# Kernel tuning notes

Measured on AMD Instinct MI355X. Metric: run time of the kernel, lower is better.

Reference implementation:

```python
import jax, jax.numpy as jnp
import numpy as np

DIM = 1152
N_HEADS = 12
GROUPS = 6
KV_HEADS = N_HEADS // GROUPS  # 2
HEAD_DIM = DIM // N_HEADS     # 96
BASE = 10000.0
BSZ = 4
SEQ = 2048
MAX_SEQ = 2048
NEG_INF = -1e9


def rope(x, start_pos):
    # x: [b, s, h, d]; interleaved (even/odd) rotary embedding, matching the torch code
    b, s, h, d = x.shape
    x_even = x[..., 0::2]
    x_odd = x[..., 1::2]
    # even positions <- -x_odd, odd positions <- x_even (interleaved)
    x_rev = jnp.stack([-x_odd, x_even], axis=-1).reshape(x.shape)
    i = jnp.repeat(jnp.arange(0, d, 2), 2).astype(x.dtype)  # [d]
    theta = 1.0 / (BASE ** (i / d))                          # [d]
    pos = jnp.arange(start_pos + s, dtype=x.dtype)           # [s] (start_pos=0 case, as in source)
    ang = pos[:, None] * theta[None, :]                      # [s, d]
    cos = jnp.cos(ang).reshape(1, s, 1, d)
    sin = jnp.sin(ang).reshape(1, s, 1, d)
    return x * cos + x_rev * sin


def setup_inputs() -> dict:
    key = jax.random.key(0)
    ks = jax.random.split(key, 4)
    sc = 0.02
    x = jax.random.normal(ks[0], (BSZ, SEQ, DIM), jnp.float32)
    # causal mask [S, end_pos]: 0 on/below diagonal, large negative above
    mask = jnp.triu(jnp.full((SEQ, SEQ), NEG_INF, jnp.float32), k=1)
    q_w = jax.random.normal(ks[1], (DIM, DIM), jnp.float32) * sc
    q_b = jnp.zeros((DIM,), jnp.float32)
    kv_w = jax.random.normal(ks[2], (2 * KV_HEADS * HEAD_DIM, DIM), jnp.float32) * sc
    kv_b = jnp.zeros((2 * KV_HEADS * HEAD_DIM,), jnp.float32)
    wo_w = jax.random.normal(ks[3], (DIM, DIM), jnp.float32) * sc
    wo_b = jnp.zeros((DIM,), jnp.float32)
    return {"x": x, "mask": mask, "q_w": q_w, "q_b": q_b, "kv_w": kv_w,
            "kv_b": kv_b, "wo_w": wo_w, "wo_b": wo_b, "start_pos": 0}


def reference(x, mask, q_w, q_b, kv_w, kv_b, wo_w, wo_b, start_pos):
    b, s, f = x.shape
    end = start_pos + s
    q = (x @ q_w.T + q_b).reshape(b, s, N_HEADS, HEAD_DIM)
    kv = (x @ kv_w.T + kv_b).reshape(b, s, 2, KV_HEADS, HEAD_DIM)
    k, v = kv[:, :, 0], kv[:, :, 1]
    rq = rope(q, start_pos)
    rk = rope(k, start_pos)
    # KV-cache write (cache initialized to zeros, as in the buffer)
    k_cache = jnp.zeros((b, MAX_SEQ, KV_HEADS, HEAD_DIM), x.dtype).at[:, start_pos:end].set(rk)
    v_cache = jnp.zeros((b, MAX_SEQ, KV_HEADS, HEAD_DIM), x.dtype).at[:, start_pos:end].set(v)
    # repeat_kv: head index = kv_head * groups + g  -> jnp.repeat along head axis
    kk = jnp.repeat(k_cache[:, :end], GROUPS, axis=2)  # [b, t, H, d]
    vv = jnp.repeat(v_cache[:, :end], GROUPS, axis=2)
    scale = HEAD_DIM ** -0.5
    attn = jnp.einsum('bshd,bthd->bsht', rq, kk) * scale
    attn = attn + mask[:, None, :]  # mask [s, t] -> [s, 1, t] broadcast over b, h
    scores = jax.nn.softmax(attn.astype(jnp.float32), axis=-1).astype(x.dtype)
    out = jnp.einsum('bsht,bthd->bshd', scores, vv).reshape(b, s, DIM)
    return out @ wo_w.T + wo_b
```

## Files before the change

kernel.cpp:

```cpp
#include <hip/hip_runtime.h>
#include <hip/hip_bf16.h>

constexpr int DIMD  = 1152;
constexpr int NHD   = 12;
constexpr int KVHD  = 2;
constexpr int HDD   = 96;
constexpr int GRPS  = 6;
constexpr int SEQL  = 2048;
constexpr int BSZ4  = 4;
constexpr int MROWS = BSZ4 * SEQL;
constexpr int NQKV  = DIMD + 2 * KVHD * HDD;
constexpr float SCALE = 0.10206207261596577f;
constexpr float SCALE2 = 0.10206207261596577f * 1.4426950408889634f;

typedef short  bf16x8 __attribute__((ext_vector_type(8)));
typedef float  f32x4  __attribute__((ext_vector_type(4)));

typedef __attribute__((address_space(3))) unsigned int       lds_u32_t;
typedef __attribute__((address_space(1))) const unsigned int glb_u32_t;

__device__ __forceinline__ void gload16(const unsigned short* g, unsigned short* l) {
    __builtin_amdgcn_global_load_lds((glb_u32_t*)(const void*)g,
                                     (lds_u32_t*)(void*)l, 16, 0, 0);
}

__device__ __forceinline__ unsigned short f2bf(float f) {
    unsigned int u = __builtin_bit_cast(unsigned int, f);
    u += 0x7fff + ((u >> 16) & 1);
    return (unsigned short)(u >> 16);
}

__device__ __forceinline__ unsigned cvtpk(float a, float b) {
    unsigned r;
    asm volatile("v_cvt_pk_bf16_f32 %0, %1, %2" : "=v"(r) : "v"(a), "v"(b));
    return r;
}

__device__ __forceinline__ float ex2(float x) {
    float r;
    asm volatile("v_exp_f32 %0, %1" : "=v"(r) : "v"(x));
    return r;
}

__device__ __forceinline__ void cvt4(const float4* __restrict__ s,
                                     ushort4* __restrict__ d, int i) {
    float4 f = s[i];
    ushort4 o;
    o.x = f2bf(f.x); o.y = f2bf(f.y); o.z = f2bf(f.z); o.w = f2bf(f.w);
    d[i] = o;
}

__global__ __launch_bounds__(256) void prep_kernel(
    const float4* __restrict__ x,   const float4* __restrict__ qw,
    const float4* __restrict__ kvw, const float4* __restrict__ wow,
    ushort4* __restrict__ xb,   ushort4* __restrict__ qwb,
    ushort4* __restrict__ kvwb, ushort4* __restrict__ wowb,
    const int* __restrict__ sp, float2* __restrict__ tab)
{
    constexpr int X4  = MROWS * DIMD / 4;
    constexpr int W4  = DIMD * DIMD / 4;
    constexpr int KV4 = 2 * KVHD * HDD * DIMD / 4;
    constexpr int NT  = SEQL * 48;
    int i = blockIdx.x * 256 + threadIdx.x;
    if (i < X4)  { cvt4(x, xb, i); return; }
    i -= X4;
    if (i < W4)  { cvt4(qw, qwb, i); return; }
    i -= W4;
    if (i < KV4) { cvt4(kvw, kvwb, i); return; }
    i -= KV4;
    if (i < W4)  { cvt4(wow, wowb, i); return; }
    i -= W4;
    if (i < NT) {
        int s = i / 48, j = i - (i / 48) * 48;
        float th = powf(10000.0f, -(float)(2 * j) / 96.0f);
        float ang = (float)(s + *sp) * th;
        float sn, cs; sincosf(ang, &sn, &cs);
        tab[i] = make_float2(cs, sn);
    }
}

__global__ __launch_bounds__(256) void qkv_mfma_kernel(
    const unsigned short* __restrict__ xb,  const unsigned short* __restrict__ qwb,
    const unsigned short* __restrict__ kvwb,
    const float* __restrict__ qb,  const float* __restrict__ kvb,
    const float2* __restrict__ tab,
    unsigned short* __restrict__ Qo, unsigned short* __restrict__ Ko,
    unsigned short* __restrict__ VTo)
{
    __shared__ __align__(16) unsigned short As[3][128 * 32];
    __shared__ __align__(16) unsigned short Bs[3][128 * 32];

    const int tid  = threadIdx.x;
    const int w    = tid >> 6;
    const int lane = tid & 63;
    const int l16  = lane & 15;
    const int quad = lane >> 4;
    const int wm   = w >> 1, wn = w & 1;

    const int flat = (int)(blockIdx.y * gridDim.x + blockIdx.x);
    const int swz  = (flat & 7) * 96 + (flat >> 3);
    const int m0   = (swz / 12) * 128;
    const int n0   = (swz % 12) * 128;

    const unsigned short* Abase = xb + (size_t)m0 * DIMD;
    const unsigned short* Bbase = (n0 < DIMD)
        ? qwb  + (size_t)n0 * DIMD
        : kvwb + (size_t)(n0 - DIMD) * DIMD;

    const int srow = w * 16 + (lane >> 2);
    const int scol = (lane & 3) * 8;

    f32x4 acc[4][4];
    #pragma unroll
    for (int mi = 0; mi < 4; mi++)
        #pragma unroll
        for (int ni = 0; ni < 4; ni++) acc[mi][ni] = (f32x4){0.f, 0.f, 0.f, 0.f};

    constexpr int NK = DIMD / 32;

    gload16(Abase + (size_t)srow        * DIMD + scol, &As[0][w * 512]);
    gload16(Abase + (size_t)(srow + 64) * DIMD + scol, &As[0][2048 + w * 512]);
    gload16(Bbase + (size_t)srow        * DIMD + scol, &Bs[0][w * 512]);
    gload16(Bbase + (size_t)(srow + 64) * DIMD + scol, &Bs[0][2048 + w * 512]);
    gload16(Abase + (size_t)srow        * DIMD + 32 + scol, &As[1][w * 512]);
    gload16(Abase + (size_t)(srow + 64) * DIMD + 32 + scol, &As[1][2048 + w * 512]);
    gload16(Bbase + (size_t)srow        * DIMD + 32 + scol, &Bs[1][w * 512]);
    gload16(Bbase + (size_t)(srow + 64) * DIMD + 32 + scol, &Bs[1][2048 + w * 512]);

    for (int kt = 0; kt < NK; kt++) {
        const int cur = kt % 3;
        if (kt + 2 < NK) {
            const int stg = (kt + 2) % 3;
            const int k0  = (kt + 2) * 32;
            gload16(Abase + (size_t)srow        * DIMD + k0 + scol, &As[stg][w * 512]);
            gload16(Abase + (size_t)(srow + 64) * DIMD + k0 + scol, &As[stg][2048 + w * 512]);
            gload16(Bbase + (size_t)srow        * DIMD + k0 + scol, &Bs[stg][w * 512]);
            gload16(Bbase + (size_t)(srow + 64) * DIMD + k0 + scol, &Bs[stg][2048 + w * 512]);
            asm volatile("s_waitcnt vmcnt(8)" ::: "memory");
        } else if (kt + 1 < NK) {
            asm volatile("s_waitcnt vmcnt(4)" ::: "memory");
        } else {
            asm volatile("s_waitcnt vmcnt(0)" ::: "memory");
        }
        __builtin_amdgcn_s_barrier();
        asm volatile("" ::: "memory");

        bf16x8 af[4], bfr[4];
        #pragma unroll
        for (int mi = 0; mi < 4; mi++)
            af[mi] = *(const bf16x8*)&As[cur][(wm * 64 + mi * 16 + l16) * 32 + quad * 8];
        #pragma unroll
        for (int ni = 0; ni < 4; ni++)
            bfr[ni] = *(const bf16x8*)&Bs[cur][(wn * 64 + ni * 16 + l16) * 32 + quad * 8];
        #pragma unroll
        for (int mi = 0; mi < 4; mi++)
            #pragma unroll
            for (int ni = 0; ni < 4; ni++)
                acc[mi][ni] = __builtin_amdgcn_mfma_f32_16x16x32_bf16(
                    af[mi], bfr[ni], acc[mi][ni], 0, 0, 0);

        asm volatile("" ::: "memory");
        __builtin_amdgcn_s_barrier();
    }

    #pragma unroll
    for (int ni = 0; ni < 4; ni++) {
        const int n   = n0 + wn * 64 + ni * 16 + l16;
        const bool isQ = (n < DIMD);
        const int jj  = n - DIMD;
        const bool isK = !isQ && (jj < KVHD * HDD);
        const int d   = isQ ? (n % HDD) : (jj % HDD);
        const int hh  = isQ ? (n / HDD) : ((jj / HDD) & 1);
        const float bias = isQ ? qb[n] : kvb[jj];
        const bool doRope = isQ || isK;
        const int de2 = (d >> 1);
        const float sg = (n & 1) ? 1.0f : -1.0f;
        #pragma unroll
        for (int mi = 0; mi < 4; mi++) {
            #pragma unroll
            for (int r = 0; r < 4; r++) {
                const int m = m0 + wm * 64 + mi * 16 + quad * 4 + r;
                const int b = m >> 11;
                const int s = m & (SEQL - 1);
                float v  = acc[mi][ni][r] + bias;
                float pv = __shfl_xor(v, 1, 64);
                float o = v;
                if (doRope) {
                    float2 cs2 = tab[s * 48 + de2];
                    o = v * cs2.x + sg * pv * cs2.y;
                }
                if (isQ)
                    Qo[(((size_t)b * NHD + hh) * SEQL + s) * HDD + d] = f2bf(o);
                else if (isK)
                    Ko[(((size_t)b * KVHD + hh) * SEQL + s) * HDD + d] = f2bf(o);
                else
                    VTo[(((size_t)b * KVHD + hh) * HDD + d) * SEQL + s] = f2bf(o);
            }
        }
    }
}

__global__ __launch_bounds__(256, 3) void attn_mfma_kernel(
    const unsigned short* __restrict__ Q, const unsigned short* __restrict__ K,
    const unsigned short* __restrict__ VT, unsigned short* __restrict__ AO)
{
    constexpr int KHALF = 64 * 104;
    __shared__ __align__(16) unsigned short Ks[2 * KHALF];
    __shared__ __align__(16) unsigned short VTs[96 * 72];
    __shared__ __align__(16) unsigned short Ps[4][16 * 72];
    __shared__ float Al[4][16];

    const int tid  = threadIdx.x;
    const int w    = tid >> 6;
    const int lane = tid & 63;
    const int l16  = lane & 15;
    const int quad = lane >> 4;

    const int idx  = (int)blockIdx.x;
    const int grp  = idx & 7;
    const int j    = idx >> 3;
    const int jq   = j / 6;
    const int hrem = j - jq * 6;
    const int qt   = 31 - jq;
    const int b    = grp >> 1;
    const int kvh  = grp & 1;
    const int h    = kvh * GRPS + hrem;
    const int nkb  = qt + 1;

    const unsigned short* Qbase  = Q  + (((size_t)b * NHD  + h)   * SEQL) * HDD;
    const unsigned short* Kbase  = K  + (((size_t)b * KVHD + kvh) * SEQL) * HDD;
    const unsigned short* VTbase = VT + (((size_t)b * KVHD + kvh) * HDD)  * SEQL;

    int goff[7]; int gkind[7]; int loff[7];
    #pragma unroll
    for (int jj = 0; jj < 7; jj++) {
        const int i = w + 4 * jj;
        gkind[jj] = 2; goff[jj] = 0; loff[jj] = 0;
        if (i < 13) {
            int slot = i * 64 + lane;
            int r = slot / 13, g = slot - r * 13;
            goff[jj]  = r * HDD + (g < 12 ? g * 8 : 0);
            gkind[jj] = 0;
            loff[jj]  = i * 512;
        } else if (i < 27) {
            int iv = i - 13;
            int slot = iv * 64 + lane;
            if (slot < 864) {
                int r = slot / 9, g = slot - r * 9;
                goff[jj]  = r * SEQL + (g < 8 ? g * 8 : 0);
                gkind[jj] = 1;
                loff[jj]  = iv * 512;
            }
        }
    }

    bf16x8 qf[3];
    {
        const int qrow = qt * 64 + w * 16 + l16;
        const unsigned short* qp = Qbase + (size_t)qrow * HDD + quad * 8;
        qf[0] = *(const bf16x8*)(qp);
        qf[1] = *(const bf16x8*)(qp + 32);
        qf[2] = *(const bf16x8*)(qp + 64);
    }

    float m_r = -1e30f, l_r = 0.0f;
    f32x4 oacc[6];
    #pragma unroll
    for (int nn = 0; nn < 6; nn++) oacc[nn] = (f32x4){0.f, 0.f, 0.f, 0.f};

    #pragma unroll
    for (int jj = 0; jj < 7; jj++)
        if (gkind[jj] == 0)
            gload16(Kbase + goff[jj], &Ks[loff[jj]]);
    #pragma unroll
    for (int jj = 0; jj < 7; jj++)
        if (gkind[jj] == 1) {
            if ((w + 4 * jj) < 26 || lane < 32)
                gload16(VTbase + goff[jj], &VTs[loff[jj]]);
        }

    const int dql = w * 16 + l16;

    for (int kb = 0; kb < nkb; kb++) {
        const int  cur  = kb & 1;
        const bool more = (kb + 1 < nkb);

        if (more) {
            const size_t kg = (size_t)(kb + 1) * 64 * HDD;
            #pragma unroll
            for (int jj = 0; jj < 7; jj++)
                if (gkind[jj] == 0)
                    gload16(Kbase + kg + goff[jj], &Ks[(cur ^ 1) * KHALF + loff[jj]]);
            asm volatile("s_waitcnt vmcnt(6)" ::: "memory");
        } else {
            asm volatile("s_waitcnt vmcnt(3)" ::: "memory");
        }
        __builtin_amdgcn_s_barrier();
        asm volatile("" ::: "memory");

        const unsigned short* ksb = &Ks[cur * KHALF];
        f32x4 s[4];
        __builtin_amdgcn_s_setprio(1);
        #pragma unroll
        for (int n = 0; n < 4; n++) {
            const unsigned short* kr = ksb + (n * 16 + l16) * 104 + quad * 8;
            bf16x8 kf0 = *(const bf16x8*)(kr);
            bf16x8 kf1 = *(const bf16x8*)(kr + 32);
            bf16x8 kf2 = *(const bf16x8*)(kr + 64);
            f32x4 a = (f32x4){0.f, 0.f, 0.f, 0.f};
            a = __builtin_amdgcn_mfma_f32_16x16x32_bf16(kf0, qf[0], a, 0, 0, 0);
            a = __builtin_amdgcn_mfma_f32_16x16x32_bf16(kf1, qf[1], a, 0, 0, 0);
            a = __builtin_amdgcn_mfma_f32_16x16x32_bf16(kf2, qf[2], a, 0, 0, 0);
            s[n] = a;
        }
        __builtin_amdgcn_s_setprio(0);

        float v[4][4];
        float mx = -3e30f;
        if (!more) {
            #pragma unroll
            for (int n = 0; n < 4; n++)
                #pragma unroll
                for (int r = 0; r < 4; r++) {
                    float x = s[n][r] * SCALE2;
                    if (n * 16 + quad * 4 + r > dql) x = -1e30f;
                    v[n][r] = x;
                    mx = fmaxf(mx, x);
                }
        } else {
            #pragma unroll
            for (int n = 0; n < 4; n++)
                #pragma unroll
                for (int r = 0; r < 4; r++) {
                    float x = s[n][r] * SCALE2;
                    v[n][r] = x;
                    mx = fmaxf(mx, x);
                }
        }
        mx = fmaxf(mx, __shfl_xor(mx, 16, 64));
        mx = fmaxf(mx, __shfl_xor(mx, 32, 64));

        const bool resc = !__all(mx <= m_r + 8.0f);
        float mnew = m_r, al = 1.0f;
        if (resc) {
            mnew = fmaxf(m_r, mx);
            al = ex2(m_r - mnew);
            if (quad == 0) Al[w][l16] = al;
        }
        float sum = 0.0f;
        #pragma unroll
        for (int n = 0; n < 4; n++) {
            float p0 = ex2(v[n][0] - mnew);
            float p1 = ex2(v[n][1] - mnew);
            float p2 = ex2(v[n][2] - mnew);
            float p3 = ex2(v[n][3] - mnew);
            sum += (p0 + p1) + (p2 + p3);
            uint2 pk;
            pk.x = cvtpk(p0, p1);
            pk.y = cvtpk(p2, p3);
            *(uint2*)&Ps[w][l16 * 72 + n * 16 + quad * 4] = pk;
        }
        sum += __shfl_xor(sum, 16, 64);
        sum += __shfl_xor(sum, 32, 64);
        l_r = l_r * al + sum;
        m_r = mnew;
        __builtin_amdgcn_wave_barrier();

        bf16x8 pa0 = *(const bf16x8*)&Ps[w][l16 * 72 + quad * 8];
        bf16x8 pa1 = *(const bf16x8*)&Ps[w][l16 * 72 + 32 + quad * 8];

        if (more) asm volatile("s_waitcnt vmcnt(3)" ::: "memory");
        else      asm volatile("s_waitcnt vmcnt(0)" ::: "memory");
        __builtin_amdgcn_s_barrier();
        asm volatile("" ::: "memory");

        if (resc) {
            const float4 alb = *(const float4*)&Al[w][quad * 4];
            const float albr[4] = {alb.x, alb.y, alb.z, alb.w};
            #pragma unroll
            for (int nn = 0; nn < 6; nn++)
                #pragma unroll
                for (int r = 0; r < 4; r++) oacc[nn][r] *= albr[r];
        }

        __builtin_amdgcn_s_setprio(1);
        #pragma unroll
        for (int nn = 0; nn < 6; nn++) {
            const unsigned short* vr = &VTs[(nn * 16 + l16) * 72 + quad * 8];
            bf16x8 vb0 = *(const bf16x8*)(vr);
            bf16x8 vb1 = *(const bf16x8*)(vr + 32);
            f32x4 a = oacc[nn];
            a = __builtin_amdgcn_mfma_f32_16x16x32_bf16(pa0, vb0, a, 0, 0, 0);
            a = __builtin_amdgcn_mfma_f32_16x16x32_bf16(pa1, vb1, a, 0, 0, 0);
            oacc[nn] = a;
        }
        __builtin_amdgcn_s_setprio(0);

        asm volatile("" ::: "memory");
        __builtin_amdgcn_s_barrier();
        asm volatile("" ::: "memory");

        if (more) {
            const int kg = (kb + 1) * 64;
            #pragma unroll
            for (int jj = 0; jj < 7; jj++)
                if (gkind[jj] == 1) {
                    if ((w + 4 * jj) < 26 || lane < 32)
                        gload16(VTbase + kg + goff[jj], &VTs[loff[jj]]);
                }
        }
    }

    const float linv = 1.0f / l_r;
    if (quad == 0) Al[w][l16] = linv;
    __builtin_amdgcn_wave_barrier();
    const float4 lb4 = *(const float4*)&Al[w][quad * 4];
    const float lbr[4] = {lb4.x, lb4.y, lb4.z, lb4.w};
    const int row0 = qt * 64 + w * 16 + quad * 4;
    #pragma unroll
    for (int nn = 0; nn < 6; nn++) {
        #pragma unroll
        for (int r = 0; r < 4; r++) {
            AO[((size_t)b * SEQL + row0 + r) * DIMD + h * HDD + nn * 16 + l16] =
                f2bf(oacc[nn][r] * lbr[r]);
        }
    }
}

__global__ __launch_bounds__(256) void out_mfma_kernel(
    const unsigned short* __restrict__ Ab, const unsigned short* __restrict__ Wb,
    const float* __restrict__ wob, float* __restrict__ out)
{
    __shared__ __align__(16) unsigned short As[3][128 * 32];
    __shared__ __align__(16) unsigned short Bs[3][128 * 32];

    const int tid  = threadIdx.x;
    const int w    = tid >> 6;
    const int lane = tid & 63;
    const int l16  = lane & 15;
    const int quad = lane >> 4;
    const int wm   = w >> 1, wn = w & 1;

    const int flat = (int)(blockIdx.y * gridDim.x + blockIdx.x);
    const int swz  = (flat & 7) * 72 + (flat >> 3);
    const int m0   = (swz / 9) * 128;
    const int n0   = (swz % 9) * 128;

    const unsigned short* Abase = Ab + (size_t)m0 * DIMD;
    const unsigned short* Bbase = Wb + (size_t)n0 * DIMD;

    const int srow = w * 16 + (lane >> 2);
    const int scol = (lane & 3) * 8;

    f32x4 acc[4][4];
    #pragma unroll
    for (int mi = 0; mi < 4; mi++)
        #pragma unroll
        for (int ni = 0; ni < 4; ni++) acc[mi][ni] = (f32x4){0.f, 0.f, 0.f, 0.f};

    constexpr int NK = DIMD / 32;

    gload16(Abase + (size_t)srow        * DIMD + scol, &As[0][w * 512]);
    gload16(Abase + (size_t)(srow + 64) * DIMD + scol, &As[0][2048 + w * 512]);
    gload16(Bbase + (size_t)srow        * DIMD + scol, &Bs[0][w * 512]);
    gload16(Bbase + (size_t)(srow + 64) * DIMD + scol, &Bs[0][2048 + w * 512]);
    gload16(Abase + (size_t)srow        * DIMD + 32 + scol, &As[1][w * 512]);
    gload16(Abase + (size_t)(srow + 64) * DIMD + 32 + scol, &As[1][2048 + w * 512]);
    gload16(Bbase + (size_t)srow        * DIMD + 32 + scol, &Bs[1][w * 512]);
    gload16(Bbase + (size_t)(srow + 64) * DIMD + 32 + scol, &Bs[1][2048 + w * 512]);

    for (int kt = 0; kt < NK; kt++) {
        const int cur = kt % 3;
        if (kt + 2 < NK) {
            const int stg = (kt + 2) % 3;
            const int k0  = (kt + 2) * 32;
            gload16(Abase + (size_t)srow        * DIMD + k0 + scol, &As[stg][w * 512]);
            gload16(Abase + (size_t)(srow + 64) * DIMD + k0 + scol, &As[stg][2048 + w * 512]);
            gload16(Bbase + (size_t)srow        * DIMD + k0 + scol, &Bs[stg][w * 512]);
            gload16(Bbase + (size_t)(srow + 64) * DIMD + k0 + scol, &Bs[stg][2048 + w * 512]);
            asm volatile("s_waitcnt vmcnt(8)" ::: "memory");
        } else if (kt + 1 < NK) {
            asm volatile("s_waitcnt vmcnt(4)" ::: "memory");
        } else {
            asm volatile("s_waitcnt vmcnt(0)" ::: "memory");
        }
        __builtin_amdgcn_s_barrier();
        asm volatile("" ::: "memory");

        bf16x8 af[4], bfr[4];
        #pragma unroll
        for (int mi = 0; mi < 4; mi++)
            af[mi] = *(const bf16x8*)&As[cur][(wm * 64 + mi * 16 + l16) * 32 + quad * 8];
        #pragma unroll
        for (int ni = 0; ni < 4; ni++)
            bfr[ni] = *(const bf16x8*)&Bs[cur][(wn * 64 + ni * 16 + l16) * 32 + quad * 8];
        #pragma unroll
        for (int mi = 0; mi < 4; mi++)
            #pragma unroll
            for (int ni = 0; ni < 4; ni++)
                acc[mi][ni] = __builtin_amdgcn_mfma_f32_16x16x32_bf16(
                    af[mi], bfr[ni], acc[mi][ni], 0, 0, 0);

        asm volatile("" ::: "memory");
        __builtin_amdgcn_s_barrier();
    }

    #pragma unroll
    for (int ni = 0; ni < 4; ni++) {
        const int n = n0 + wn * 64 + ni * 16 + l16;
        const float bias = wob[n];
        #pragma unroll
        for (int mi = 0; mi < 4; mi++) {
            #pragma unroll
            for (int r = 0; r < 4; r++) {
                const int m = m0 + wm * 64 + mi * 16 + quad * 4 + r;
                out[(size_t)m * DIMD + n] = acc[mi][ni][r] + bias;
            }
        }
    }
}

extern "C" void kernel_launch(void* const* d_in, const int* in_sizes, int n_in,
                              void* d_out, int out_size, void* d_ws, size_t ws_size,
                              hipStream_t stream)
{
    const float* x   = (const float*)d_in[0];
    const float* qw  = (const float*)d_in[2];
    const float* qb  = (const float*)d_in[3];
    const float* kvw = (const float*)d_in[4];
    const float* kvb = (const float*)d_in[5];
    const float* wow = (const float*)d_in[6];
    const float* wob = (const float*)d_in[7];
    const int*   sp  = (const int*)d_in[8];

    const size_t xN   = (size_t)MROWS * DIMD;
    const size_t qwN  = (size_t)DIMD * DIMD;
    const size_t kvwN = (size_t)2 * KVHD * HDD * DIMD;
    const size_t qN   = (size_t)BSZ4 * NHD  * SEQL * HDD;
    const size_t kvN  = (size_t)BSZ4 * KVHD * SEQL * HDD;

    unsigned short* xb   = (unsigned short*)d_ws;
    unsigned short* qwb  = xb   + xN;
    unsigned short* kvwb = qwb  + qwN;
    unsigned short* wowb = kvwb + kvwN;
    unsigned short* Q16  = wowb + qwN;
    unsigned short* K16  = Q16  + qN;
    unsigned short* VT16 = K16  + kvN;
    unsigned short* AO16 = VT16 + kvN;
    float2* tab = (float2*)AO16;

    constexpr int PREP_TOT = (MROWS * DIMD + 2 * DIMD * DIMD
                              + 2 * KVHD * HDD * DIMD) / 4 + SEQL * 48;
    prep_kernel<<<(PREP_TOT + 255) / 256, 256, 0, stream>>>(
        (const float4*)x, (const float4*)qw, (const float4*)kvw, (const float4*)wow,
        (ushort4*)xb, (ushort4*)qwb, (ushort4*)kvwb, (ushort4*)wowb, sp, tab);

    qkv_mfma_kernel<<<dim3(NQKV / 128, MROWS / 128, 1), 256, 0, stream>>>(
        xb, qwb, kvwb, qb, kvb, tab, Q16, K16, VT16);
    attn_mfma_kernel<<<dim3((SEQL / 64) * NHD * BSZ4, 1, 1), 256, 0, stream>>>(
        Q16, K16, VT16, AO16);
    out_mfma_kernel<<<dim3(DIMD / 128, MROWS / 128, 1), 256, 0, stream>>>(
        AO16, wowb, wob, (float*)d_out);
}
```

Before: 284.8 us.

## Switch attention to 32x32x16 MFMA with split-K waves and register P

Rewrites the attention inner loop to use 32x32x16 bf16 MFMAs. Each pair of waves shares a 32-row query slice and splits the 64-key block into two 32-key halves; a wave whose half lies entirely above the causal diagonal skips its work. P is repacked into MFMA operand layout in registers with cross-lane shuffles instead of going through LDS. The two halves' partial softmax states and outputs are merged at the end through LDS, which adds an epilogue reduction and extra synchronisation. It also raises register pressure under the 3-blocks-per-CU launch bound.

After: 285.1 us, median of 2. About the same (+0.1%).

```diff
diff --git a/kernel.cpp b/kernel.cpp
--- a/kernel.cpp
+++ b/kernel.cpp
@@ -15,6 +15,8 @@
 
 typedef short  bf16x8 __attribute__((ext_vector_type(8)));
 typedef float  f32x4  __attribute__((ext_vector_type(4)));
+typedef float  f32x16 __attribute__((ext_vector_type(16)));
+typedef unsigned int u32x4_t __attribute__((ext_vector_type(4)));
 
 typedef __attribute__((address_space(3))) unsigned int       lds_u32_t;
 typedef __attribute__((address_space(1))) const unsigned int glb_u32_t;
@@ -207,20 +209,22 @@
     constexpr int KHALF = 64 * 104;
     __shared__ __align__(16) unsigned short Ks[2 * KHALF];
     __shared__ __align__(16) unsigned short VTs[96 * 72];
-    __shared__ __align__(16) unsigned short Ps[4][16 * 72];
-    __shared__ float Al[4][16];
+    __shared__ float Al[4][32];
 
     const int tid  = threadIdx.x;
     const int w    = tid >> 6;
     const int lane = tid & 63;
-    const int l16  = lane & 15;
-    const int quad = lane >> 4;
+    const int l31  = lane & 31;
+    const int hi   = lane >> 5;
+    const int qh   = w >> 1;
+    const int th   = w & 1;
+    const int th32 = th * 32;
 
     const int idx  = (int)blockIdx.x;
     const int grp  = idx & 7;
-    const int j    = idx >> 3;
-    const int jq   = j / 6;
-    const int hrem = j - jq * 6;
+    const int j0   = idx >> 3;
+    const int jq   = j0 / 6;
+    const int hrem = j0 - jq * 6;
     const int qt   = 31 - jq;
     const int b    = grp >> 1;
     const int kvh  = grp & 1;
@@ -254,19 +258,20 @@
         }
     }
 
-    bf16x8 qf[3];
+    const int qv = qt * 64 + qh * 32;
+    bf16x8 qf[6];
     {
-        const int qrow = qt * 64 + w * 16 + l16;
-        const unsigned short* qp = Qbase + (size_t)qrow * HDD + quad * 8;
-        qf[0] = *(const bf16x8*)(qp);
-        qf[1] = *(const bf16x8*)(qp + 32);
-        qf[2] = *(const bf16x8*)(qp + 64);
+        const unsigned short* qp = Qbase + (size_t)(qv + l31) * HDD + hi * 8;
+        #pragma unroll
+        for (int ks = 0; ks < 6; ks++) qf[ks] = *(const bf16x8*)(qp + ks * 16);
     }
 
     float m_r = -1e30f, l_r = 0.0f;
-    f32x4 oacc[6];
-    #pragma unroll
-    for (int nn = 0; nn < 6; nn++) oacc[nn] = (f32x4){0.f, 0.f, 0.f, 0.f};
+    f32x16 oacc[3];
+    #pragma unroll
+    for (int nn = 0; nn < 3; nn++)
+        #pragma unroll
+        for (int r = 0; r < 16; r++) oacc[nn][r] = 0.0f;
 
     #pragma unroll
     for (int jj = 0; jj < 7; jj++)
@@ -279,11 +284,11 @@
                 gload16(VTbase + goff[jj], &VTs[loff[jj]]);
         }
 
-    const int dql = w * 16 + l16;
-
     for (int kb = 0; kb < nkb; kb++) {
         const int  cur  = kb & 1;
         const bool more = (kb + 1 < nkb);
+        const int  k0   = kb * 64;
+        const bool active = (k0 + th32 <= qv + 31);
 
         if (more) {
             const size_t kg = (size_t)(kb + 1) * 64 * HDD;
@@ -298,103 +303,107 @@
         __builtin_amdgcn_s_barrier();
         asm volatile("" ::: "memory");
 
-        const unsigned short* ksb = &Ks[cur * KHALF];
-        f32x4 s[4];
-        __builtin_amdgcn_s_setprio(1);
-        #pragma unroll
-        for (int n = 0; n < 4; n++) {
-            const unsigned short* kr = ksb + (n * 16 + l16) * 104 + quad * 8;
-            bf16x8 kf0 = *(const bf16x8*)(kr);
-            bf16x8 kf1 = *(const bf16x8*)(kr + 32);
-            bf16x8 kf2 = *(const bf16x8*)(kr + 64);
-            f32x4 a = (f32x4){0.f, 0.f, 0.f, 0.f};
-            a = __builtin_amdgcn_mfma_f32_16x16x32_bf16(kf0, qf[0], a, 0, 0, 0);
-            a = __builtin_amdgcn_mfma_f32_16x16x32_bf16(kf1, qf[1], a, 0, 0, 0);
-            a = __builtin_amdgcn_mfma_f32_16x16x32_bf16(kf2, qf[2], a, 0, 0, 0);
-            s[n] = a;
-        }
-        __builtin_amdgcn_s_setprio(0);
-
-        float v[4][4];
-        float mx = -3e30f;
-        if (!more) {
-            #pragma unroll
-            for (int n = 0; n < 4; n++)
-                #pragma unroll
-                for (int r = 0; r < 4; r++) {
-                    float x = s[n][r] * SCALE2;
-                    if (n * 16 + quad * 4 + r > dql) x = -1e30f;
-                    v[n][r] = x;
-                    mx = fmaxf(mx, x);
-                }
-        } else {
-            #pragma unroll
-            for (int n = 0; n < 4; n++)
-                #pragma unroll
-                for (int r = 0; r < 4; r++) {
-                    float x = s[n][r] * SCALE2;
-                    v[n][r] = x;
-                    mx = fmaxf(mx, x);
-                }
-        }
-        mx = fmaxf(mx, __shfl_xor(mx, 16, 64));
-        mx = fmaxf(mx, __shfl_xor(mx, 32, 64));
-
-        const bool resc = !__all(mx <= m_r + 8.0f);
-        float mnew = m_r, al = 1.0f;
-        if (resc) {
-            mnew = fmaxf(m_r, mx);
-            al = ex2(m_r - mnew);
-            if (quad == 0) Al[w][l16] = al;
-        }
-        float sum = 0.0f;
-        #pragma unroll
-        for (int n = 0; n < 4; n++) {
-            float p0 = ex2(v[n][0] - mnew);
-            float p1 = ex2(v[n][1] - mnew);
-            float p2 = ex2(v[n][2] - mnew);
-            float p3 = ex2(v[n][3] - mnew);
-            sum += (p0 + p1) + (p2 + p3);
-            uint2 pk;
-            pk.x = cvtpk(p0, p1);
-            pk.y = cvtpk(p2, p3);
-            *(uint2*)&Ps[w][l16 * 72 + n * 16 + quad * 4] = pk;
-        }
-        sum += __shfl_xor(sum, 16, 64);
-        sum += __shfl_xor(sum, 32, 64);
-        l_r = l_r * al + sum;
-        m_r = mnew;
-        __builtin_amdgcn_wave_barrier();
-
-        bf16x8 pa0 = *(const bf16x8*)&Ps[w][l16 * 72 + quad * 8];
-        bf16x8 pa1 = *(const bf16x8*)&Ps[w][l16 * 72 + 32 + quad * 8];
+        bf16x8 pa[2];
+        bool resc = false;
+
+        if (active) {
+            const unsigned short* ksb = &Ks[cur * KHALF + th32 * 104];
+            f32x16 s;
+            #pragma unroll
+            for (int r = 0; r < 16; r++) s[r] = 0.0f;
+            __builtin_amdgcn_s_setprio(1);
+            #pragma unroll
+            for (int ks = 0; ks < 6; ks++) {
+                bf16x8 kf = *(const bf16x8*)&ksb[l31 * 104 + ks * 16 + hi * 8];
+                s = __builtin_amdgcn_mfma_f32_32x32x16_bf16(kf, qf[ks], s, 0, 0, 0);
+            }
+            __builtin_amdgcn_s_setprio(0);
+
+            const int qabs = qv + l31;
+            float p[16];
+            float mx = -3e30f;
+            const bool domask = (k0 + th32 + 31 > qv);
+            #pragma unroll
+            for (int r = 0; r < 16; r++) {
+                const int tl = (r & 3) + 8 * (r >> 2) + 4 * hi;
+                float x = s[r] * SCALE2;
+                if (domask && (k0 + th32 + tl > qabs)) x = -1e30f;
+                p[r] = x;
+                mx = fmaxf(mx, x);
+            }
+            mx = fmaxf(mx, __shfl_xor(mx, 32, 64));
+
+            resc = !__all(mx <= m_r + 8.0f);
+            float mnew = m_r, al = 1.0f;
+            if (resc) {
+                mnew = fmaxf(m_r, mx);
+                al = ex2(m_r - mnew);
+                if (hi == 0) Al[w][l31] = al;
+            }
+            float sum = 0.0f;
+            #pragma unroll
+            for (int r = 0; r < 16; r++) {
+                p[r] = ex2(p[r] - mnew);
+                sum += p[r];
+            }
+            sum += __shfl_xor(sum, 32, 64);
+            l_r = l_r * al + sum;
+            m_r = mnew;
+
+            #pragma unroll
+            for (int tk = 0; tk < 2; tk++) {
+                const int base = tk * 8;
+                unsigned pkA0 = cvtpk(p[base + 0], p[base + 1]);
+                unsigned pkA1 = cvtpk(p[base + 2], p[base + 3]);
+                unsigned pkB0 = cvtpk(p[base + 4], p[base + 5]);
+                unsigned pkB1 = cvtpk(p[base + 6], p[base + 7]);
+                unsigned S0 = hi ? pkA0 : pkB0;
+                unsigned S1 = hi ? pkA1 : pkB1;
+                unsigned R0 = __shfl_xor(S0, 32, 64);
+                unsigned R1 = __shfl_xor(S1, 32, 64);
+                u32x4_t wv;
+                wv[0] = hi ? R0 : pkA0;
+                wv[1] = hi ? R1 : pkA1;
+                wv[2] = hi ? pkB0 : R0;
+                wv[3] = hi ? pkB1 : R1;
+                pa[tk] = __builtin_bit_cast(bf16x8, wv);
+            }
+        }
 
         if (more) asm volatile("s_waitcnt vmcnt(3)" ::: "memory");
         else      asm volatile("s_waitcnt vmcnt(0)" ::: "memory");
         __builtin_amdgcn_s_barrier();
         asm volatile("" ::: "memory");
 
-        if (resc) {
-            const float4 alb = *(const float4*)&Al[w][quad * 4];
-            const float albr[4] = {alb.x, alb.y, alb.z, alb.w};
-            #pragma unroll
-            for (int nn = 0; nn < 6; nn++)
+        if (active) {
+            if (resc) {
+                const float4 a0 = *(const float4*)&Al[w][hi * 4];
+                const float4 a1 = *(const float4*)&Al[w][8 + hi * 4];
+                const float4 a2 = *(const float4*)&Al[w][16 + hi * 4];
+                const float4 a3 = *(const float4*)&Al[w][24 + hi * 4];
+                const float ab[16] = {a0.x, a0.y, a0.z, a0.w,
+                                      a1.x, a1.y, a1.z, a1.w,
+                                      a2.x, a2.y, a2.z, a2.w,
+                                      a3.x, a3.y, a3.z, a3.w};
                 #pragma unroll
-                for (int r = 0; r < 4; r++) oacc[nn][r] *= albr[r];
-        }
-
-        __builtin_amdgcn_s_setprio(1);
-        #pragma unroll
-        for (int nn = 0; nn < 6; nn++) {
-            const unsigned short* vr = &VTs[(nn * 16 + l16) * 72 + quad * 8];
-            bf16x8 vb0 = *(const bf16x8*)(vr);
-            bf16x8 vb1 = *(const bf16x8*)(vr + 32);
-            f32x4 a = oacc[nn];
-            a = __builtin_amdgcn_mfma_f32_16x16x32_bf16(pa0, vb0, a, 0, 0, 0);
-            a = __builtin_amdgcn_mfma_f32_16x16x32_bf16(pa1, vb1, a, 0, 0, 0);
-            oacc[nn] = a;
-        }
-        __builtin_amdgcn_s_setprio(0);
+                for (int nn = 0; nn < 3; nn++)
+                    #pragma unroll
+                    for (int r = 0; r < 16; r++) oacc[nn][r] *= ab[r];
+            }
+
+            __builtin_amdgcn_s_setprio(1);
+            #pragma unroll
+            for (int nn = 0; nn < 3; nn++) {
+                const unsigned short* vr = &VTs[(nn * 32 + l31) * 72 + th32 + hi * 8];
+                bf16x8 vb0 = *(const bf16x8*)(vr);
+                bf16x8 vb1 = *(const bf16x8*)(vr + 16);
+                f32x16 a = oacc[nn];
+                a = __builtin_amdgcn_mfma_f32_32x32x16_bf16(pa[0], vb0, a, 0, 0, 0);
+                a = __builtin_amdgcn_mfma_f32_32x32x16_bf16(pa[1], vb1, a, 0, 0, 0);
+                oacc[nn] = a;
+            }
+            __builtin_amdgcn_s_setprio(0);
+        }
 
         asm volatile("" ::: "memory");
         __builtin_amdgcn_s_barrier();
@@ -411,19 +420,60 @@
         }
     }
 
-    const float linv = 1.0f / l_r;
-    if (quad == 0) Al[w][l16] = linv;
-    __builtin_amdgcn_wave_barrier();
-    const float4 lb4 = *(const float4*)&Al[w][quad * 4];
-    const float lbr[4] = {lb4.x, lb4.y, lb4.z, lb4.w};
-    const int row0 = qt * 64 + w * 16 + quad * 4;
-    #pragma unroll
-    for (int nn = 0; nn < 6; nn++) {
-        #pragma unroll
-        for (int r = 0; r < 4; r++) {
-            AO[((size_t)b * SEQL + row0 + r) * DIMD + h * HDD + nn * 16 + l16] =
-                f2bf(oacc[nn][r] * lbr[r]);
-        }
+    __syncthreads();
+    float* Mx  = (float*)VTs;
+    float* Lx  = Mx + 128;
+    float* Gs  = Lx + 128;
+    float* Osc = (float*)Ks;
+    if (hi == 0) { Mx[w * 32 + l31] = m_r; Lx[w * 32 + l31] = l_r; }
+    __syncthreads();
+    {
+        const int wp = w ^ 1;
+        const float m_p = Mx[wp * 32 + l31];
+        const float l_p = Lx[wp * 32 + l31];
+        const float mm  = fmaxf(m_r, m_p);
+        const float fs  = ex2(m_r - mm);
+        const float lt  = l_r * fs + l_p * ex2(m_p - mm);
+        if (hi == 0) Gs[w * 32 + l31] = fs / lt;
+    }
+    __syncthreads();
+    float gr[16];
+    {
+        const float4 a0 = *(const float4*)&Gs[w * 32 + hi * 4];
+        const float4 a1 = *(const float4*)&Gs[w * 32 + 8 + hi * 4];
+        const float4 a2 = *(const float4*)&Gs[w * 32 + 16 + hi * 4];
+        const float4 a3 = *(const float4*)&Gs[w * 32 + 24 + hi * 4];
+        gr[0]  = a0.x; gr[1]  = a0.y; gr[2]  = a0.z; gr[3]  = a0.w;
+        gr[4]  = a1.x; gr[5]  = a1.y; gr[6]  = a1.z; gr[7]  = a1.w;
+        gr[8]  = a2.x; gr[9]  = a2.y; gr[10] = a2.z; gr[11] = a2.w;
+        gr[12] = a3.x; gr[13] = a3.y; gr[14] = a3.z; gr[15] = a3.w;
+    }
+    #pragma unroll
+    for (int nn = 0; nn < 3; nn++)
+        #pragma unroll
+        for (int r = 0; r < 16; r++) oacc[nn][r] *= gr[r];
+
+    if (th == 1) {
+        #pragma unroll
+        for (int nn = 0; nn < 3; nn++)
+            #pragma unroll
+            for (int r = 0; r < 16; r++) {
+                const int ql = (r & 3) + 8 * (r >> 2) + 4 * hi;
+                Osc[(qh * 32 + ql) * 96 + nn * 32 + l31] = oacc[nn][r];
+            }
+    }
+    __syncthreads();
+    if (th == 0) {
+        #pragma unroll
+        for (int nn = 0; nn < 3; nn++)
+            #pragma unroll
+            for (int r = 0; r < 16; r++) {
+                const int ql = (r & 3) + 8 * (r >> 2) + 4 * hi;
+                const float v2 = oacc[nn][r]
+                               + Osc[(qh * 32 + ql) * 96 + nn * 32 + l31];
+                AO[((size_t)b * SEQL + qv + ql) * DIMD + h * HDD + nn * 32 + l31]
+                    = f2bf(v2);
+            }
     }
 }
 
```
